# Performance work log

Hardware: AMD Instinct MI355X
Metric: run time of the kernel (lower is better)

## Reference

```python
import jax, jax.numpy as jnp
import numpy as np

ALPHA = 0.2  # LeakyReLU slope
NEG = -1e9


def setup_inputs() -> dict:
    key = jax.random.key(0)
    k1, k2, k3, k4, k5 = jax.random.split(key, 5)
    B, N, F_IN, F_OUT, H = 8, 1024, 512, 256, 8
    x = jax.random.normal(k1, (B, N, F_IN), dtype=jnp.float32)
    adj = jax.random.randint(k2, (B, N, N), 0, 2, dtype=jnp.int32)
    W = jax.random.normal(k3, (H, F_OUT, F_IN), dtype=jnp.float32) * 0.05
    a1 = jax.random.normal(k4, (H, F_OUT), dtype=jnp.float32) * 0.05
    a2 = jax.random.normal(k5, (H, F_OUT), dtype=jnp.float32) * 0.05
    return {"x": x, "adj": adj, "W": W, "a1": a1, "a2": a2}


def _head(x, adj_zero, W, a1, a2):
    # x: (B,N,F_in), W: (F_out,F_in), a1/a2: (F_out,)
    h = jnp.einsum('bnf,of->bno', x, W)              # (B,N,F_out)
    f1 = jnp.einsum('bno,o->bn', h, a1)              # (B,N)
    f2 = jnp.einsum('bno,o->bn', h, a2)              # (B,N)
    e = f1[:, :, None] + f2[:, None, :]              # (B,N,N) broadcast add
    e = jax.nn.leaky_relu(e, negative_slope=ALPHA)
    e = jnp.where(adj_zero, NEG, e)                  # adjacency mask
    att = jax.nn.softmax(e, axis=2)
    return jnp.einsum('bnm,bmo->bno', att, h)        # (B,N,F_out)


def reference(x, adj, W, a1, a2):
    adj_zero = (adj == 0)
    # vmap over heads; sum of elu(head outputs)
    heads = jax.vmap(lambda w, u, v: _head(x, adj_zero, w, u, v))(W, a1, a2)  # (H,B,N,F_out)
    out = jnp.sum(jax.nn.elu(heads), axis=0)         # (B,N,F_out)
    return jax.nn.log_softmax(out, axis=2)
```

## Files before the change

kernel.cpp:

```cpp
#include <hip/hip_runtime.h>
#include <math.h>

#define B_    8
#define N_    1024
#define FIN   512
#define FOUT  256
#define H_    8
#define ALPHA 0.2f

#define XT (B_ * N_ * FIN)
#define WT (H_ * FOUT * FIN)

typedef short s16x8 __attribute__((ext_vector_type(8)));
typedef float f32x4 __attribute__((ext_vector_type(4)));

__device__ __forceinline__ unsigned short f2bf(float f) {
  unsigned int u = __float_as_uint(f);
  u = (u + 0x7FFFu + ((u >> 16) & 1u)) >> 16;
  return (unsigned short)u;
}

__device__ __forceinline__ unsigned int pk4_fp8(float a, float b, float c,
                                                float d) {
  int u = __builtin_amdgcn_cvt_pk_fp8_f32(a, b, 0, false);
  u = __builtin_amdgcn_cvt_pk_fp8_f32(c, d, u, true);
  return (unsigned int)u;
}


#define CVB  ((XT + WT) / 1024)
#define ZRB  128
#define PKB  ((B_ * N_ * 32) / 256)

__global__ __launch_bounds__(256) void prep(
    const float* __restrict__ x, const float* __restrict__ W,
    const int* __restrict__ adj, unsigned short* __restrict__ xb,
    unsigned short* __restrict__ Wb, float* __restrict__ f12,
    unsigned int* __restrict__ adjP) {
  const int blk = blockIdx.x;
  if (blk >= CVB + ZRB) {
    const int dw = (blk - CVB - ZRB) * 256 + threadIdx.x;
    const int r = dw >> 5, pd = dw & 31;
    const int q = pd >> 3, c8 = pd & 7;
    const int* ap = adj + (size_t)r * N_;
    unsigned int out = 0;
#pragma unroll
    for (int i = 0; i < 4; ++i) {
      const int jb = (c8 * 4 + i) * 32 + q * 8;
      int4 v0 = *(const int4*)(ap + jb);
      int4 v1 = *(const int4*)(ap + jb + 4);
      unsigned int byte = 0;
      byte |= (v0.x ? 1u : 0u) << 0; byte |= (v0.y ? 1u : 0u) << 1;
      byte |= (v0.z ? 1u : 0u) << 2; byte |= (v0.w ? 1u : 0u) << 3;
      byte |= (v1.x ? 1u : 0u) << 4; byte |= (v1.y ? 1u : 0u) << 5;
      byte |= (v1.z ? 1u : 0u) << 6; byte |= (v1.w ? 1u : 0u) << 7;
      out |= byte << (i * 8);
    }
    adjP[dw] = out;
    return;
  }
  if (blk >= CVB) {
    const int i = (blk - CVB) * 256 + threadIdx.x;
    ((float4*)f12)[i] = make_float4(0.f, 0.f, 0.f, 0.f);
    return;
  }
  const int i = (blk * 256 + threadIdx.x) * 4;
  const float* src;
  unsigned short* dst;
  int off;
  if (i < XT) { src = x; dst = xb; off = i; }
  else        { src = W; dst = Wb; off = i - XT; }
  float4 v = *(const float4*)(src + off);
  ushort4 s;
  s.x = f2bf(v.x); s.y = f2bf(v.y); s.z = f2bf(v.z); s.w = f2bf(v.w);
  *(ushort4*)(dst + off) = s;
}

__global__ __launch_bounds__(256) void proj_mfma(
    const unsigned short* __restrict__ xb, const unsigned short* __restrict__ Wb,
    const float* __restrict__ a1, const float* __restrict__ a2,
    unsigned char* __restrict__ htq, float* __restrict__ f1,
    float* __restrict__ f2) {
  __shared__ __align__(16) unsigned short As[128 * 64];
  __shared__ __align__(16) unsigned short Bs[64 * 64];
  const int gid = blockIdx.x;
  const int b = gid & 7;
  const int mt_ = (gid >> 3) & 7;
  const int ot_ = (gid >> 6) & 3;
  const int h = gid >> 8;
  const int hb = h * B_ + b;
  const int m0 = mt_ * 128, o0 = ot_ * 64;
  const int t = threadIdx.x, w = t >> 6, lane = t & 63;
  const int col = lane & 15, quad = lane >> 4;

  const int srow = t >> 3;
  const int sslot = t & 7;
  const int sseg = sslot ^ (srow & 7);
  const unsigned short* agp = xb + (size_t)(b * N_ + m0 + srow) * FIN + sseg * 8;
  const unsigned short* bgp = Wb + (size_t)(h * FOUT + o0 + srow) * FIN + sseg * 8;

  f32x4 acc[2][4];
  const f32x4 z4 = {0.f, 0.f, 0.f, 0.f};
#pragma unroll
  for (int mt = 0; mt < 2; ++mt)
#pragma unroll
    for (int ot = 0; ot < 4; ++ot) acc[mt][ot] = z4;

  s16x8 pa[4], pb[2];
#pragma unroll
  for (int i2 = 0; i2 < 4; ++i2) pa[i2] = *(const s16x8*)(agp + (size_t)i2 * 32 * FIN);
#pragma unroll
  for (int i2 = 0; i2 < 2; ++i2) pb[i2] = *(const s16x8*)(bgp + (size_t)i2 * 32 * FIN);

  for (int it = 0; it < FIN / 64; ++it) {
    __syncthreads();
#pragma unroll
    for (int i2 = 0; i2 < 4; ++i2)
      *(s16x8*)&As[(i2 * 32 + srow) * 64 + sslot * 8] = pa[i2];
#pragma unroll
    for (int i2 = 0; i2 < 2; ++i2)
      *(s16x8*)&Bs[(i2 * 32 + srow) * 64 + sslot * 8] = pb[i2];
    __syncthreads();
    if (it < FIN / 64 - 1) {
      const int k0 = (it + 1) * 64;
#pragma unroll
      for (int i2 = 0; i2 < 4; ++i2)
        pa[i2] = *(const s16x8*)(agp + (size_t)i2 * 32 * FIN + k0);
#pragma unroll
      for (int i2 = 0; i2 < 2; ++i2)
        pb[i2] = *(const s16x8*)(bgp + (size_t)i2 * 32 * FIN + k0);
    }
#pragma unroll
    for (int kb = 0; kb < 2; ++kb) {
      s16x8 af[2], bf[4];
#pragma unroll
      for (int mt = 0; mt < 2; ++mt) {
        const int row = w * 32 + mt * 16 + col;
        af[mt] = *(const s16x8*)&As[row * 64 + ((kb * 4 + quad) ^ (row & 7)) * 8];
      }
#pragma unroll
      for (int ot = 0; ot < 4; ++ot) {
        const int row = ot * 16 + col;
        bf[ot] = *(const s16x8*)&Bs[row * 64 + ((kb * 4 + quad) ^ (row & 7)) * 8];
      }
#pragma unroll
      for (int mt = 0; mt < 2; ++mt)
#pragma unroll
        for (int ot = 0; ot < 4; ++ot)
          acc[mt][ot] = __builtin_amdgcn_mfma_f32_16x16x32_bf16(af[mt], bf[ot],
                                                                acc[mt][ot], 0, 0, 0);
    }
  }

  const int kkw = (m0 >> 5) + w;
  float pf1[2][4] = {{0.f}}, pf2[2][4] = {{0.f}};
#pragma unroll
  for (int mt = 0; mt < 2; ++mt) {
#pragma unroll
    for (int ot = 0; ot < 4; ++ot) {
      const int o = o0 + ot * 16 + col;
      const float va1 = a1[h * FOUT + o], va2 = a2[h * FOUT + o];
      const int otg = (o0 >> 4) + ot;
      unsigned char* fb =
          htq + (((size_t)(hb * 16 + otg) * 32 + kkw) << 9);
      const unsigned int q =
          pk4_fp8(acc[mt][ot][0], acc[mt][ot][1], acc[mt][ot][2], acc[mt][ot][3]);
      *(unsigned int*)(fb + (2 * mt + (quad >> 1)) * 128 + col * 8 +
                       (quad & 1) * 4) = q;
#pragma unroll
      for (int r = 0; r < 4; ++r) {
        pf1[mt][r] += acc[mt][ot][r] * va1;
        pf2[mt][r] += acc[mt][ot][r] * va2;
      }
    }
  }
#pragma unroll
  for (int off = 1; off <= 8; off <<= 1)
#pragma unroll
    for (int mt = 0; mt < 2; ++mt)
#pragma unroll
      for (int r = 0; r < 4; ++r) {
        pf1[mt][r] += __shfl_xor(pf1[mt][r], off);
        pf2[mt][r] += __shfl_xor(pf2[mt][r], off);
      }
  if (col == 0) {
#pragma unroll
    for (int mt = 0; mt < 2; ++mt)
#pragma unroll
      for (int r = 0; r < 4; ++r) {
        const int n = m0 + w * 32 + mt * 16 + quad * 4 + r;
        atomicAdd(&f1[hb * N_ + n], pf1[mt][r]);
        atomicAdd(&f2[hb * N_ + n], pf2[mt][r]);
      }
  }
}

__global__ __launch_bounds__(256) void wgen(
    const float* __restrict__ f1, const float* __restrict__ f2,
    const unsigned int* __restrict__ adjP, unsigned char* __restrict__ wq) {
  const int id = blockIdx.x;
  const int b = id & 7, h = (id >> 3) & 7;
  const int rbg = (id >> 6) & 15;
  const int kkh = id >> 10;
  const int w = threadIdx.x >> 6, lane = threadIdx.x & 63;
  const int col = lane & 15, quad = lane >> 4;
  const int hb = h * B_ + b;
  const int rb = rbg * 4 + w;
  const int row = rb * 16 + col;

  const float* f2r = f2 + (size_t)hb * N_;
  float m2 = -3.0e38f;
#pragma unroll
  for (int c = 0; c < 16; ++c) m2 = fmaxf(m2, f2r[lane + c * 64]);
#pragma unroll
  for (int off = 32; off; off >>= 1) m2 = fmaxf(m2, __shfl_xor(m2, off));

  const float f1i = f1[(size_t)hb * N_ + row];
  const float tb = f1i + m2;
  const float mhat = fmaxf(tb, ALPHA * tb);

  const unsigned int* adp = adjP + ((size_t)(b * N_ + row) << 5) + quad * 8;
  const float* f2p = f2r + quad * 8;
  unsigned char* wp = wq + (((size_t)(hb * 64 + rb) * 32) << 9) + lane * 8;

#pragma unroll
  for (int k4i = 0; k4i < 4; ++k4i) {
    const int k4 = kkh * 4 + k4i;
    const unsigned int ad = adp[k4];
#pragma unroll
    for (int k2 = 0; k2 < 4; ++k2) {
      const int kk = k4 * 4 + k2;
      const unsigned int ab = (ad >> (k2 * 8)) & 0xFFu;
      const float4 fA = *(const float4*)(f2p + kk * 32);
      const float4 fB = *(const float4*)(f2p + kk * 32 + 4);
      float ex[8];
#pragma unroll
      for (int j = 0; j < 8; ++j) {
        const float fv = j < 4 ? ((const float*)&fA)[j]
                               : ((const float*)&fB)[j - 4];
        const float tt = f1i + fv;
        const float l = fmaxf(tt, ALPHA * tt);
        const float p = __expf(l - mhat);
        ex[j] = ((ab >> j) & 1u) ? p : 0.f;
      }
      const unsigned int lo = pk4_fp8(ex[0], ex[1], ex[2], ex[3]);
      const unsigned int hi = pk4_fp8(ex[4], ex[5], ex[6], ex[7]);
      *(uint2*)(wp + kk * 512) = make_uint2(lo, hi);
    }
  }
}

__global__ __launch_bounds__(256, 4) void pv(
    const unsigned char* __restrict__ htq, const unsigned char* __restrict__ wq,
    float* __restrict__ p0, float* __restrict__ p1, float* __restrict__ p2,
    float* __restrict__ p3) {
  const int id = blockIdx.x;
  const int b = id & 7;
  const int g0 = (id >> 3) & 3;
  const int oq = (id >> 5) & 3;
  const int it = id >> 7;
  const int w = threadIdx.x >> 6, lane = threadIdx.x & 63;
  const int col = lane & 15, quad = lane >> 4;
  const int rb = it * 8 + w * 2;

  float hsum[2][4][4];
#pragma unroll
  for (int g = 0; g < 2; ++g)
#pragma unroll
    for (int t = 0; t < 4; ++t)
#pragma unroll
      for (int r = 0; r < 4; ++r) hsum[g][t][r] = 0.f;

  const long ones = 0x3838383838383838L;

  for (int hh = 0; hh < 2; ++hh) {
    const int hb = (g0 * 2 + hh) * B_ + b;
    const unsigned char* ap =
        wq + (((size_t)(hb * 64 + rb) * 32) << 9) + lane * 8;
    const unsigned char* bp =
        htq + (((size_t)(hb * 16 + oq * 4) * 32) << 9) + lane * 8;

    f32x4 acc[2][4], accs[2];
    const f32x4 z4 = {0.f, 0.f, 0.f, 0.f};
#pragma unroll
    for (int g = 0; g < 2; ++g) {
      accs[g] = z4;
#pragma unroll
      for (int t = 0; t < 4; ++t) acc[g][t] = z4;
    }

#pragma unroll 2
    for (int kk = 0; kk < 32; ++kk) {
      const long af0 = *(const long*)(ap + kk * 512);
      const long af1 = *(const long*)(ap + 16384 + kk * 512);
      accs[0] = __builtin_amdgcn_mfma_f32_16x16x32_fp8_fp8(af0, ones, accs[0], 0, 0, 0);
      accs[1] = __builtin_amdgcn_mfma_f32_16x16x32_fp8_fp8(af1, ones, accs[1], 0, 0, 0);
#pragma unroll
      for (int t = 0; t < 4; ++t) {
        const long bf = *(const long*)(bp + ((t * 32 + kk) << 9));
        acc[0][t] = __builtin_amdgcn_mfma_f32_16x16x32_fp8_fp8(af0, bf,
                                                               acc[0][t], 0, 0, 0);
        acc[1][t] = __builtin_amdgcn_mfma_f32_16x16x32_fp8_fp8(af1, bf,
                                                               acc[1][t], 0, 0, 0);
      }
    }

#pragma unroll
    for (int g = 0; g < 2; ++g)
#pragma unroll
      for (int r = 0; r < 4; ++r) {
        const float inv = 1.0f / accs[g][r];
#pragma unroll
        for (int t = 0; t < 4; ++t) {
          const float oh = acc[g][t][r] * inv;
          hsum[g][t][r] += oh > 0.f ? oh : __expf(oh) - 1.f;
        }
      }
  }

  float* pdst = (g0 == 0) ? p0 : (g0 == 1) ? p1 : (g0 == 2) ? p2 : p3;
#pragma unroll
  for (int g = 0; g < 2; ++g)
#pragma unroll
    for (int t = 0; t < 4; ++t)
#pragma unroll
      for (int r = 0; r < 4; ++r) {
        const int orow = (rb + g) * 16 + quad * 4 + r;
        pdst[(size_t)(b * N_ + orow) * FOUT + oq * 64 + t * 16 + col] =
            hsum[g][t][r];
      }
}

__global__ __launch_bounds__(256) void logsm(
    const float* __restrict__ p0, const float* __restrict__ p1,
    const float* __restrict__ p2, const float* __restrict__ p3,
    float* __restrict__ out) {
  const int row = blockIdx.x * 4 + (threadIdx.x >> 6);
  const int lane = threadIdx.x & 63;
  const size_t base = (size_t)row * FOUT;
  float v[4];
  float m = -3.0e38f;
#pragma unroll
  for (int c = 0; c < 4; ++c) {
    const size_t idx = base + c * 64 + lane;
    v[c] = p0[idx] + p1[idx] + p2[idx] + p3[idx];
    m = fmaxf(m, v[c]);
  }
#pragma unroll
  for (int off = 32; off; off >>= 1) m = fmaxf(m, __shfl_xor(m, off));
  float s = 0.f;
#pragma unroll
  for (int c = 0; c < 4; ++c) s += __expf(v[c] - m);
#pragma unroll
  for (int off = 32; off; off >>= 1) s += __shfl_xor(s, off);
  const float lg = m + logf(s);
#pragma unroll
  for (int c = 0; c < 4; ++c)
    out[base + c * 64 + lane] = v[c] - lg;
}

extern "C" void kernel_launch(void* const* d_in, const int* in_sizes, int n_in,
                              void* d_out, int out_size, void* d_ws,
                              size_t ws_size, hipStream_t stream) {
  const float* x   = (const float*)d_in[0];
  const int*   adj = (const int*)d_in[1];
  const float* W   = (const float*)d_in[2];
  const float* a1  = (const float*)d_in[3];
  const float* a2  = (const float*)d_in[4];
  float* out = (float*)d_out;

  unsigned char* htq = (unsigned char*)d_ws;
  unsigned short* xb = (unsigned short*)(htq + (size_t)H_ * B_ * FOUT * N_);
  unsigned short* Wb = xb + (size_t)XT;
  float* f1 = (float*)(Wb + (size_t)WT);
  float* f2 = f1 + (size_t)H_ * B_ * N_;
  float* part2 = f2 + (size_t)H_ * B_ * N_;
  float* part3 = part2 + (size_t)B_ * N_ * FOUT;
  unsigned int* adjP = (unsigned int*)(part3 + (size_t)B_ * N_ * FOUT);
  unsigned char* wq = (unsigned char*)(adjP + (size_t)B_ * N_ * 32);
  float* part1 = (float*)xb;

  prep<<<CVB + ZRB + PKB, 256, 0, stream>>>(x, W, adj, xb, Wb, f1, adjP);

  proj_mfma<<<2048, 256, 0, stream>>>(xb, Wb, a1, a2, htq, f1, f2);

  wgen<<<2048, 256, 0, stream>>>(f1, f2, adjP, wq);

  pv<<<1024, 256, 0, stream>>>(htq, wq, out, part1, part2, part3);

  logsm<<<(B_ * N_) / 4, 256, 0, stream>>>(out, part1, part2, part3, out);
}
```

Before: 210.4 us.

## Pre-swizzle x and W into MFMA fragment layout and drop LDS staging in projection

The prep kernel now writes the bf16-converted x and W directly in the per-lane MFMA fragment order, with each 16x32 tile stored as a contiguous 1KB block. The projection GEMM then loads its A and B fragments straight from global memory with 16-byte loads and no shared memory or block barriers. Each wave computes a 32x64 output tile independently. This removes the LDS round trip and __syncthreads, but gives up shared-memory reuse of B across waves and relies on L2/L1 caching for repeated fragment loads.

```diff
diff --git a/kernel.cpp b/kernel.cpp
--- a/kernel.cpp
+++ b/kernel.cpp
@@ -28,169 +28,158 @@
 }
 
 
-#define CVB  ((XT + WT) / 1024)
+#define XQB  2048
+#define WQB  512
 #define ZRB  128
 #define PKB  ((B_ * N_ * 32) / 256)
 
 __global__ __launch_bounds__(256) void prep(
     const float* __restrict__ x, const float* __restrict__ W,
-    const int* __restrict__ adj, unsigned short* __restrict__ xb,
-    unsigned short* __restrict__ Wb, float* __restrict__ f12,
+    const int* __restrict__ adj, unsigned short* __restrict__ xq,
+    unsigned short* __restrict__ Wq, float* __restrict__ f12,
     unsigned int* __restrict__ adjP) {
   const int blk = blockIdx.x;
-  if (blk >= CVB + ZRB) {
-    const int dw = (blk - CVB - ZRB) * 256 + threadIdx.x;
-    const int r = dw >> 5, pd = dw & 31;
-    const int q = pd >> 3, c8 = pd & 7;
-    const int* ap = adj + (size_t)r * N_;
-    unsigned int out = 0;
-#pragma unroll
-    for (int i = 0; i < 4; ++i) {
-      const int jb = (c8 * 4 + i) * 32 + q * 8;
-      int4 v0 = *(const int4*)(ap + jb);
-      int4 v1 = *(const int4*)(ap + jb + 4);
-      unsigned int byte = 0;
-      byte |= (v0.x ? 1u : 0u) << 0; byte |= (v0.y ? 1u : 0u) << 1;
-      byte |= (v0.z ? 1u : 0u) << 2; byte |= (v0.w ? 1u : 0u) << 3;
-      byte |= (v1.x ? 1u : 0u) << 4; byte |= (v1.y ? 1u : 0u) << 5;
-      byte |= (v1.z ? 1u : 0u) << 6; byte |= (v1.w ? 1u : 0u) << 7;
-      out |= byte << (i * 8);
-    }
-    adjP[dw] = out;
+  const int w = threadIdx.x >> 6, l = threadIdx.x & 63;
+  const int col = l & 15, qd = l >> 4;
+
+  if (blk < XQB) {
+    const int wv = blk * 4 + w;
+    const int b = wv >> 10, rest = wv & 1023;
+    const int mb = rest >> 4, fb = rest & 15;
+    const float* src = x + ((size_t)(b * N_ + mb * 16 + col)) * FIN +
+                       fb * 32 + qd * 8;
+    float4 v0 = *(const float4*)src;
+    float4 v1 = *(const float4*)(src + 4);
+    s16x8 sv;
+    sv[0] = (short)f2bf(v0.x); sv[1] = (short)f2bf(v0.y);
+    sv[2] = (short)f2bf(v0.z); sv[3] = (short)f2bf(v0.w);
+    sv[4] = (short)f2bf(v1.x); sv[5] = (short)f2bf(v1.y);
+    sv[6] = (short)f2bf(v1.z); sv[7] = (short)f2bf(v1.w);
+    *(s16x8*)((unsigned char*)xq +
+              (((size_t)(b * 64 + mb) * 16 + fb) << 10) + l * 16) = sv;
     return;
   }
-  if (blk >= CVB) {
-    const int i = (blk - CVB) * 256 + threadIdx.x;
+  if (blk < XQB + WQB) {
+    const int wv = (blk - XQB) * 4 + w;
+    const int h = wv >> 8, rest = wv & 255;
+    const int otg = rest >> 4, fb = rest & 15;
+    const float* src = W + ((size_t)(h * FOUT + otg * 16 + col)) * FIN +
+                       fb * 32 + qd * 8;
+    float4 v0 = *(const float4*)src;
+    float4 v1 = *(const float4*)(src + 4);
+    s16x8 sv;
+    sv[0] = (short)f2bf(v0.x); sv[1] = (short)f2bf(v0.y);
+    sv[2] = (short)f2bf(v0.z); sv[3] = (short)f2bf(v0.w);
+    sv[4] = (short)f2bf(v1.x); sv[5] = (short)f2bf(v1.y);
+    sv[6] = (short)f2bf(v1.z); sv[7] = (short)f2bf(v1.w);
+    *(s16x8*)((unsigned char*)Wq +
+              (((size_t)(h * 16 + otg) * 16 + fb) << 10) + l * 16) = sv;
+    return;
+  }
+  if (blk < XQB + WQB + ZRB) {
+    const int i = (blk - XQB - WQB) * 256 + threadIdx.x;
     ((float4*)f12)[i] = make_float4(0.f, 0.f, 0.f, 0.f);
     return;
   }
-  const int i = (blk * 256 + threadIdx.x) * 4;
-  const float* src;
-  unsigned short* dst;
-  int off;
-  if (i < XT) { src = x; dst = xb; off = i; }
-  else        { src = W; dst = Wb; off = i - XT; }
-  float4 v = *(const float4*)(src + off);
-  ushort4 s;
-  s.x = f2bf(v.x); s.y = f2bf(v.y); s.z = f2bf(v.z); s.w = f2bf(v.w);
-  *(ushort4*)(dst + off) = s;
+  const int dw = (blk - XQB - WQB - ZRB) * 256 + threadIdx.x;
+  const int r = dw >> 5, pd = dw & 31;
+  const int q = pd >> 3, c8 = pd & 7;
+  const int* ap = adj + (size_t)r * N_;
+  unsigned int out = 0;
+#pragma unroll
+  for (int i = 0; i < 4; ++i) {
+    const int jb = (c8 * 4 + i) * 32 + q * 8;
+    int4 v0 = *(const int4*)(ap + jb);
+    int4 v1 = *(const int4*)(ap + jb + 4);
+    unsigned int byte = 0;
+    byte |= (v0.x ? 1u : 0u) << 0; byte |= (v0.y ? 1u : 0u) << 1;
+    byte |= (v0.z ? 1u : 0u) << 2; byte |= (v0.w ? 1u : 0u) << 3;
+    byte |= (v1.x ? 1u : 0u) << 4; byte |= (v1.y ? 1u : 0u) << 5;
+    byte |= (v1.z ? 1u : 0u) << 6; byte |= (v1.w ? 1u : 0u) << 7;
+    out |= byte << (i * 8);
+  }
+  adjP[dw] = out;
 }
 
 __global__ __launch_bounds__(256) void proj_mfma(
-    const unsigned short* __restrict__ xb, const unsigned short* __restrict__ Wb,
+    const unsigned short* __restrict__ xq, const unsigned short* __restrict__ Wq,
     const float* __restrict__ a1, const float* __restrict__ a2,
     unsigned char* __restrict__ htq, float* __restrict__ f1,
     float* __restrict__ f2) {
-  __shared__ __align__(16) unsigned short As[128 * 64];
-  __shared__ __align__(16) unsigned short Bs[64 * 64];
-  const int gid = blockIdx.x;
-  const int b = gid & 7;
-  const int mt_ = (gid >> 3) & 7;
-  const int ot_ = (gid >> 6) & 3;
-  const int h = gid >> 8;
+  const int blk = blockIdx.x;
+  const int b = blk & 7;
+  const int h = (blk >> 3) & 7;
+  const int oq = (blk >> 6) & 3;
+  const int mgg = blk >> 8;
+  const int w = threadIdx.x >> 6, l = threadIdx.x & 63;
+  const int col = l & 15, quad = l >> 4;
+  const int mg = mgg * 4 + w;
   const int hb = h * B_ + b;
-  const int m0 = mt_ * 128, o0 = ot_ * 64;
-  const int t = threadIdx.x, w = t >> 6, lane = t & 63;
-  const int col = lane & 15, quad = lane >> 4;
-
-  const int srow = t >> 3;
-  const int sslot = t & 7;
-  const int sseg = sslot ^ (srow & 7);
-  const unsigned short* agp = xb + (size_t)(b * N_ + m0 + srow) * FIN + sseg * 8;
-  const unsigned short* bgp = Wb + (size_t)(h * FOUT + o0 + srow) * FIN + sseg * 8;
+
+  const unsigned char* ap = (const unsigned char*)xq +
+      (((size_t)(b * 64 + mg * 2) * 16) << 10) + l * 16;
+  const unsigned char* bp = (const unsigned char*)Wq +
+      (((size_t)(h * 16 + oq * 4) * 16) << 10) + l * 16;
 
   f32x4 acc[2][4];
   const f32x4 z4 = {0.f, 0.f, 0.f, 0.f};
 #pragma unroll
-  for (int mt = 0; mt < 2; ++mt)
-#pragma unroll
-    for (int ot = 0; ot < 4; ++ot) acc[mt][ot] = z4;
-
-  s16x8 pa[4], pb[2];
-#pragma unroll
-  for (int i2 = 0; i2 < 4; ++i2) pa[i2] = *(const s16x8*)(agp + (size_t)i2 * 32 * FIN);
-#pragma unroll
-  for (int i2 = 0; i2 < 2; ++i2) pb[i2] = *(const s16x8*)(bgp + (size_t)i2 * 32 * FIN);
-
-  for (int it = 0; it < FIN / 64; ++it) {
-    __syncthreads();
-#pragma unroll
-    for (int i2 = 0; i2 < 4; ++i2)
-      *(s16x8*)&As[(i2 * 32 + srow) * 64 + sslot * 8] = pa[i2];
-#pragma unroll
-    for (int i2 = 0; i2 < 2; ++i2)
-      *(s16x8*)&Bs[(i2 * 32 + srow) * 64 + sslot * 8] = pb[i2];
-    __syncthreads();
-    if (it < FIN / 64 - 1) {
-      const int k0 = (it + 1) * 64;
-#pragma unroll
-      for (int i2 = 0; i2 < 4; ++i2)
-        pa[i2] = *(const s16x8*)(agp + (size_t)i2 * 32 * FIN + k0);
-#pragma unroll
-      for (int i2 = 0; i2 < 2; ++i2)
-        pb[i2] = *(const s16x8*)(bgp + (size_t)i2 * 32 * FIN + k0);
-    }
-#pragma unroll
-    for (int kb = 0; kb < 2; ++kb) {
-      s16x8 af[2], bf[4];
-#pragma unroll
-      for (int mt = 0; mt < 2; ++mt) {
-        const int row = w * 32 + mt * 16 + col;
-        af[mt] = *(const s16x8*)&As[row * 64 + ((kb * 4 + quad) ^ (row & 7)) * 8];
-      }
-#pragma unroll
-      for (int ot = 0; ot < 4; ++ot) {
-        const int row = ot * 16 + col;
-        bf[ot] = *(const s16x8*)&Bs[row * 64 + ((kb * 4 + quad) ^ (row & 7)) * 8];
-      }
-#pragma unroll
-      for (int mt = 0; mt < 2; ++mt)
-#pragma unroll
-        for (int ot = 0; ot < 4; ++ot)
-          acc[mt][ot] = __builtin_amdgcn_mfma_f32_16x16x32_bf16(af[mt], bf[ot],
-                                                                acc[mt][ot], 0, 0, 0);
-    }
-  }
-
-  const int kkw = (m0 >> 5) + w;
+  for (int g = 0; g < 2; ++g)
+#pragma unroll
+    for (int t = 0; t < 4; ++t) acc[g][t] = z4;
+
+#pragma unroll 4
+  for (int fb = 0; fb < 16; ++fb) {
+    const s16x8 af0 = *(const s16x8*)(ap + (fb << 10));
+    const s16x8 af1 = *(const s16x8*)(ap + 16384 + (fb << 10));
+#pragma unroll
+    for (int t = 0; t < 4; ++t) {
+      const s16x8 bf = *(const s16x8*)(bp + (((t * 16) + fb) << 10));
+      acc[0][t] = __builtin_amdgcn_mfma_f32_16x16x32_bf16(af0, bf, acc[0][t],
+                                                          0, 0, 0);
+      acc[1][t] = __builtin_amdgcn_mfma_f32_16x16x32_bf16(af1, bf, acc[1][t],
+                                                          0, 0, 0);
+    }
+  }
+
   float pf1[2][4] = {{0.f}}, pf2[2][4] = {{0.f}};
 #pragma unroll
-  for (int mt = 0; mt < 2; ++mt) {
-#pragma unroll
-    for (int ot = 0; ot < 4; ++ot) {
-      const int o = o0 + ot * 16 + col;
+  for (int g = 0; g < 2; ++g) {
+#pragma unroll
+    for (int t = 0; t < 4; ++t) {
+      const int o = (oq * 4 + t) * 16 + col;
       const float va1 = a1[h * FOUT + o], va2 = a2[h * FOUT + o];
-      const int otg = (o0 >> 4) + ot;
-      unsigned char* fb =
-          htq + (((size_t)(hb * 16 + otg) * 32 + kkw) << 9);
-      const unsigned int q =
-          pk4_fp8(acc[mt][ot][0], acc[mt][ot][1], acc[mt][ot][2], acc[mt][ot][3]);
-      *(unsigned int*)(fb + (2 * mt + (quad >> 1)) * 128 + col * 8 +
-                       (quad & 1) * 4) = q;
-#pragma unroll
-      for (int r = 0; r < 4; ++r) {
-        pf1[mt][r] += acc[mt][ot][r] * va1;
-        pf2[mt][r] += acc[mt][ot][r] * va2;
+      const int otg = oq * 4 + t;
+      unsigned char* fb_out =
+          htq + (((size_t)(hb * 16 + otg) * 32 + mg) << 9);
+      const unsigned int qv =
+          pk4_fp8(acc[g][t][0], acc[g][t][1], acc[g][t][2], acc[g][t][3]);
+      *(unsigned int*)(fb_out + (g * 2 + (quad >> 1)) * 128 + col * 8 +
+                       (quad & 1) * 4) = qv;
+#pragma unroll
+      for (int r = 0; r < 4; ++r) {
+        pf1[g][r] += acc[g][t][r] * va1;
+        pf2[g][r] += acc[g][t][r] * va2;
       }
     }
   }
 #pragma unroll
   for (int off = 1; off <= 8; off <<= 1)
 #pragma unroll
-    for (int mt = 0; mt < 2; ++mt)
-#pragma unroll
-      for (int r = 0; r < 4; ++r) {
-        pf1[mt][r] += __shfl_xor(pf1[mt][r], off);
-        pf2[mt][r] += __shfl_xor(pf2[mt][r], off);
+    for (int g = 0; g < 2; ++g)
+#pragma unroll
+      for (int r = 0; r < 4; ++r) {
+        pf1[g][r] += __shfl_xor(pf1[g][r], off);
+        pf2[g][r] += __shfl_xor(pf2[g][r], off);
       }
   if (col == 0) {
 #pragma unroll
-    for (int mt = 0; mt < 2; ++mt)
-#pragma unroll
-      for (int r = 0; r < 4; ++r) {
-        const int n = m0 + w * 32 + mt * 16 + quad * 4 + r;
-        atomicAdd(&f1[hb * N_ + n], pf1[mt][r]);
-        atomicAdd(&f2[hb * N_ + n], pf2[mt][r]);
+    for (int g = 0; g < 2; ++g)
+#pragma unroll
+      for (int r = 0; r < 4; ++r) {
+        const int n = mg * 32 + g * 16 + quad * 4 + r;
+        atomicAdd(&f1[hb * N_ + n], pf1[g][r]);
+        atomicAdd(&f2[hb * N_ + n], pf2[g][r]);
       }
   }
 }
@@ -370,19 +359,19 @@
   float* out = (float*)d_out;
 
   unsigned char* htq = (unsigned char*)d_ws;
-  unsigned short* xb = (unsigned short*)(htq + (size_t)H_ * B_ * FOUT * N_);
-  unsigned short* Wb = xb + (size_t)XT;
-  float* f1 = (float*)(Wb + (size_t)WT);
+  unsigned short* xq = (unsigned short*)(htq + (size_t)H_ * B_ * FOUT * N_);
+  unsigned short* Wq = xq + (size_t)XT;
+  float* f1 = (float*)(Wq + (size_t)WT);
   float* f2 = f1 + (size_t)H_ * B_ * N_;
   float* part2 = f2 + (size_t)H_ * B_ * N_;
   float* part3 = part2 + (size_t)B_ * N_ * FOUT;
   unsigned int* adjP = (unsigned int*)(part3 + (size_t)B_ * N_ * FOUT);
   unsigned char* wq = (unsigned char*)(adjP + (size_t)B_ * N_ * 32);
-  float* part1 = (float*)xb;
-
-  prep<<<CVB + ZRB + PKB, 256, 0, stream>>>(x, W, adj, xb, Wb, f1, adjP);
-
-  proj_mfma<<<2048, 256, 0, stream>>>(xb, Wb, a1, a2, htq, f1, f2);
+  float* part1 = (float*)xq;
+
+  prep<<<XQB + WQB + ZRB + PKB, 256, 0, stream>>>(x, W, adj, xq, Wq, f1, adjP);
+
+  proj_mfma<<<2048, 256, 0, stream>>>(xq, Wq, a1, a2, htq, f1, f2);
 
   wgen<<<2048, 256, 0, stream>>>(f1, f2, adjP, wq);
 
```

Measured after the change: 214.3 us. Within noise of the previous version (+1.8%).
